# Kernel optimization log

Measured on AMD Instinct MI355X. Metric: run time of the kernel, lower is better.

## Reference

```python
import jax, jax.numpy as jnp
import numpy as np

CHANNELS = 32


def _mlp(x, W1, b1, W2, b2, W3, b3):
    # FNN: Linear -> ReLU -> Linear -> ReLU -> Linear (last layer linear)
    h = jax.nn.relu(x @ W1 + b1)
    h = jax.nn.relu(h @ W2 + b2)
    return h @ W3 + b3


def setup_inputs() -> dict:
    key = jax.random.key(0)
    ks = jax.random.split(key, 8)
    E = 262144
    C = CHANNELS
    H = 128
    d_in = 4  # 2 * spatial_dim
    d_out = C * (C + 1)  # 1056
    s = lambda fan_in: 1.0 / np.sqrt(fan_in)
    return {
        "pos_i": jax.random.normal(ks[0], (E, 2), jnp.float32),
        "pos_j": jax.random.normal(ks[1], (E, 2), jnp.float32),
        "v_j": jax.random.normal(ks[2], (E, C), jnp.float32),
        "W1": jax.random.normal(ks[3], (d_in, H), jnp.float32) * s(d_in),
        "b1": jnp.zeros((H,), jnp.float32),
        "W2": jax.random.normal(ks[4], (H, H), jnp.float32) * s(H),
        "b2": jnp.zeros((H,), jnp.float32),
        "W3": jax.random.normal(ks[5], (H, d_out), jnp.float32) * s(H),
        "b3": jnp.zeros((d_out,), jnp.float32),
    }


def reference(pos_i, pos_j, v_j, W1, b1, W2, b2, W3, b3):
    C = CHANNELS
    pos_ij = jnp.concatenate((pos_i, pos_j), axis=-1)          # [E, 2*spatial_dim]
    kernel = _mlp(pos_ij, W1, b1, W2, b2, W3, b3)
    kernel = kernel.reshape(-1, C, C + 1)                      # [E, C, C+1]
    mat, bias = kernel[..., :, :-1], kernel[..., :, -1]        # [E,C,C], [E,C]
    return jnp.einsum('eij,ej->ei', mat, v_j) + bias           # [E, C]
```

## Files before the change

kernel.cpp:

```cpp
#include <hip/hip_runtime.h>


#define E_TOTAL 262144
#define EPB 256
#define NBLK (E_TOTAL / EPB)

typedef float f32x4 __attribute__((ext_vector_type(4)));
typedef short s8v  __attribute__((ext_vector_type(8)));
typedef short s4v  __attribute__((ext_vector_type(4)));
typedef unsigned int u32;

__device__ __forceinline__ unsigned short f2bf(float x) {
  unsigned u = __float_as_uint(x);
  u += 0x7fffu + ((u >> 16) & 1u);
  return (unsigned short)(u >> 16);
}

__device__ __forceinline__ void ld16_g2l(const void* g, void* l) {
  __builtin_amdgcn_global_load_lds((const __attribute__((address_space(1))) u32*)g,
                                   (__attribute__((address_space(3))) u32*)l, 16, 0, 0);
}

__global__ void prep_pack(const float* __restrict__ W2, const float* __restrict__ W3,
                          const float* __restrict__ b3,
                          unsigned short* __restrict__ Wg2, unsigned short* __restrict__ W2f,
                          unsigned short* __restrict__ b3f, float* __restrict__ b3c) {
  int idx = blockIdx.x * 256 + threadIdx.x;
  if (idx < 135168) {
    int k = idx / 1056, c = idx % 1056;
    int i = c / 33, jc = c % 33;
    int col = jc * 32 + i;
    int nnt = col >> 4, low = col & 15;
    int nn = (nnt & 1) ? (33 + (nnt >> 1)) : (nnt >> 1);
    int ks = k >> 5, kr = k & 31;
    int lane = ((kr >> 3) << 4) + low;
    int jj = k & 7;
    Wg2[((nn * 4 + ks) * 64 + lane) * 8 + jj] = f2bf(W3[idx]);
  }
  if (idx < 16384) {
    int k = idx >> 7, n = idx & 127;
    int ks = k >> 5, kr = k & 31;
    int nt = n >> 4, low = n & 15;
    int l = ((kr >> 3) << 4) + low;
    int jj = k & 7;
    W2f[((ks * 8 + nt) * 64 + l) * 8 + jj] = f2bf(W2[idx]);
  }
  if (idx < 1024) {
    int jj = idx & 7, lane = (idx >> 3) & 63, ih = idx >> 9;
    int j = ((lane >> 4) << 3) + jj, i = ih * 16 + (lane & 15);
    b3f[idx] = f2bf(b3[i * 33 + j]);
  }
  if (idx < 32) b3c[idx] = b3[idx * 33 + 32];
}

template <int IH>
__device__ __forceinline__ void tile_compute(const unsigned short* __restrict__ buf, int t,
                                             const float* __restrict__ vt, int j,
                                             int w, int q, int lane,
                                             const s8v (&af)[2][4], float (&oa)[2][2][4]) {
  const f32x4 zero4 = {0.f, 0.f, 0.f, 0.f};
  s8v bfr[4];
#pragma unroll
  for (int ks = 0; ks < 4; ++ks)
    bfr[ks] = *(const s8v*)&buf[(t * 4 + ks) * 512 + lane * 8];
  const float* vp = vt + j * 260 + w * 32 + q * 4;
#pragma unroll
  for (int m = 0; m < 2; ++m) {
    f32x4 p = __builtin_amdgcn_mfma_f32_16x16x32_bf16(af[m][0], bfr[0], zero4, 0, 0, 0);
#pragma unroll
    for (int ks = 1; ks < 4; ++ks)
      p = __builtin_amdgcn_mfma_f32_16x16x32_bf16(af[m][ks], bfr[ks], p, 0, 0, 0);
    f32x4 vv = *(const f32x4*)(vp + m * 16);
#pragma unroll
    for (int r = 0; r < 4; ++r) oa[IH][m][r] += vv[r] * p[r];
  }
}

__global__ __launch_bounds__(512, 4) void fnn_fused(
    const float* __restrict__ pos_i, const float* __restrict__ pos_j,
    const float* __restrict__ vj, const float* __restrict__ W1,
    const float* __restrict__ b1, const float* __restrict__ b2,
    const unsigned short* __restrict__ W2f, const unsigned short* __restrict__ Wg2,
    const unsigned short* __restrict__ b3f, const float* __restrict__ b3c,
    float* __restrict__ out) {
  __shared__ __attribute__((aligned(16))) char smem[51200];
  float* vt = (float*)smem;
  unsigned short* h1c = (unsigned short*)smem;
  unsigned short* h2n = (unsigned short*)(smem + 17408);
  unsigned short* Bb  = (unsigned short*)(smem + 34816);
  char* BbChar = smem + 34816;

  const int tid = threadIdx.x;
  const int w = tid >> 6, lane = tid & 63, q = lane >> 4, ln = lane & 15;
  const int B0 = blockIdx.x * EPB;

  const int hh0 = (tid & 31) * 4;
  float w1r[4][4], b1r4[4];
#pragma unroll
  for (int d = 0; d < 4; ++d)
#pragma unroll
    for (int u = 0; u < 4; ++u) w1r[d][u] = W1[d * 128 + hh0 + u];
#pragma unroll
  for (int u = 0; u < 4; ++u) b1r4[u] = b1[hh0 + u];

  s8v af[2][4];
  for (int qtr = 0; qtr < 4; ++qtr) {
#pragma unroll
    for (int half = 0; half < 4; ++half) {
      int ee = (tid >> 5) + half * 16;
      int eg = B0 + qtr * 64 + ee;
      float2 pi = *(const float2*)(pos_i + (size_t)eg * 2);
      float2 pj = *(const float2*)(pos_j + (size_t)eg * 2);
      s4v hv;
#pragma unroll
      for (int u = 0; u < 4; ++u) {
        float o = b1r4[u] + pi.x * w1r[0][u] + pi.y * w1r[1][u] +
                  pj.x * w1r[2][u] + pj.y * w1r[3][u];
        hv[u] = (short)f2bf(fmaxf(o, 0.f));
      }
      *(s4v*)&h1c[ee * 136 + hh0] = hv;
    }
    __syncthreads();

#pragma unroll
    for (int s = 0; s < 4; ++s) {
      int tt = w * 4 + s, mt = tt >> 3, nt = tt & 7;
      f32x4 a4 = {0.f, 0.f, 0.f, 0.f};
#pragma unroll
      for (int ks = 0; ks < 4; ++ks) {
        s8v afr = *(const s8v*)&h1c[(mt * 16 + ln) * 136 + ks * 32 + q * 8];
        s8v bfr = *(const s8v*)(W2f + ((ks * 8 + nt) * 64 + lane) * 8);
        a4 = __builtin_amdgcn_mfma_f32_16x16x32_bf16(afr, bfr, a4, 0, 0, 0);
      }
      float b2v = b2[nt * 16 + ln];
      int eb = mt * 16 + q * 4;
      int kc = nt * 16 + ln;
#pragma unroll
      for (int r = 0; r < 4; ++r)
        h2n[(eb + r) * 136 + kc] = f2bf(fmaxf(a4[r] + b2v, 0.f));
    }
    __syncthreads();

    if ((w >> 1) == qtr) {
#pragma unroll
      for (int m = 0; m < 2; ++m)
#pragma unroll
        for (int ks = 0; ks < 4; ++ks)
          af[m][ks] = *(const s8v*)&h2n[(((w & 1) * 32 + m * 16 + ln)) * 136 + ks * 32 + q * 8];
    }
  }

  {
    const unsigned short* src = Wg2 + tid * 8;
    char* dstb = BbChar + w * 1024;
    ld16_g2l(src, dstb);
  }
  __syncthreads();

  float oa[2][2][4];
  {
    s8v av[2];
#pragma unroll
    for (int m = 0; m < 2; ++m) {
      int e = B0 + w * 32 + m * 16 + ln;
      const float4 va = *(const float4*)(vj + (size_t)e * 32 + q * 8);
      const float4 vb = *(const float4*)(vj + (size_t)e * 32 + q * 8 + 4);
      s8v t;
      t[0] = (short)f2bf(va.x); t[1] = (short)f2bf(va.y);
      t[2] = (short)f2bf(va.z); t[3] = (short)f2bf(va.w);
      t[4] = (short)f2bf(vb.x); t[5] = (short)f2bf(vb.y);
      t[6] = (short)f2bf(vb.z); t[7] = (short)f2bf(vb.w);
      av[m] = t;
    }
#pragma unroll
    for (int ih = 0; ih < 2; ++ih) {
      s8v b3fr = *(const s8v*)(b3f + (ih * 64 + lane) * 8);
      float cbv = b3c[ih * 16 + ln];
      f32x4 ci = {cbv, cbv, cbv, cbv};
#pragma unroll
      for (int m = 0; m < 2; ++m) {
        f32x4 p = __builtin_amdgcn_mfma_f32_16x16x32_bf16(av[m], b3fr, ci, 0, 0, 0);
#pragma unroll
        for (int r = 0; r < 4; ++r) oa[ih][m][r] = p[r];
      }
    }
  }

  if (tid < 256) {
    const float* vrow = vj + (size_t)(B0 + tid) * 32;
#pragma unroll
    for (int j4 = 0; j4 < 8; ++j4) {
      float4 vv = *(const float4*)(vrow + j4 * 4);
      vt[(j4 * 4 + 0) * 260 + tid] = vv.x;
      vt[(j4 * 4 + 1) * 260 + tid] = vv.y;
      vt[(j4 * 4 + 2) * 260 + tid] = vv.z;
      vt[(j4 * 4 + 3) * 260 + tid] = vv.w;
    }
    vt[32 * 260 + tid] = 1.0f;
  }
  __syncthreads();

#pragma unroll 1
  for (int c = 0; c < 16; ++c) {
    const unsigned short* buf = Bb + (c & 1) * 4096;
    {
      const unsigned short* src = Wg2 + (size_t)(c + 1) * 4096 + tid * 8;
      char* dstb = BbChar + ((c + 1) & 1) * 8192 + w * 1024;
      ld16_g2l(src, dstb);
    }
    tile_compute<0>(buf, 0, vt, 2 * c,     w, q, lane, af, oa);
    tile_compute<0>(buf, 1, vt, 2 * c + 1, w, q, lane, af, oa);
    __syncthreads();
  }
  {
    const unsigned short* buf = Bb;
    {
      const unsigned short* src = Wg2 + (size_t)17 * 4096 + tid * 8;
      char* dstb = BbChar + 8192 + w * 1024;
      ld16_g2l(src, dstb);
    }
    tile_compute<0>(buf, 0, vt, 32, w, q, lane, af, oa);
    tile_compute<1>(buf, 1, vt, 0,  w, q, lane, af, oa);
    __syncthreads();
  }
#pragma unroll 1
  for (int c = 17; c < 33; ++c) {
    const unsigned short* buf = Bb + (c & 1) * 4096;
    if (c < 32) {
      const unsigned short* src = Wg2 + (size_t)(c + 1) * 4096 + tid * 8;
      char* dstb = BbChar + ((c + 1) & 1) * 8192 + w * 1024;
      ld16_g2l(src, dstb);
    }
    tile_compute<1>(buf, 0, vt, 2 * c - 33, w, q, lane, af, oa);
    tile_compute<1>(buf, 1, vt, 2 * c - 32, w, q, lane, af, oa);
    __syncthreads();
  }

#pragma unroll
  for (int m = 0; m < 2; ++m)
#pragma unroll
    for (int ih = 0; ih < 2; ++ih)
#pragma unroll
      for (int r = 0; r < 4; ++r) {
        int e = B0 + w * 32 + m * 16 + q * 4 + r;
        out[(size_t)e * 32 + ih * 16 + ln] = oa[ih][m][r];
      }
}

extern "C" void kernel_launch(void* const* d_in, const int* in_sizes, int n_in,
                              void* d_out, int out_size, void* d_ws, size_t ws_size,
                              hipStream_t stream) {
  const float* pos_i = (const float*)d_in[0];
  const float* pos_j = (const float*)d_in[1];
  const float* vj    = (const float*)d_in[2];
  const float* W1    = (const float*)d_in[3];
  const float* b1    = (const float*)d_in[4];
  const float* W2    = (const float*)d_in[5];
  const float* b2    = (const float*)d_in[6];
  const float* W3    = (const float*)d_in[7];
  const float* b3    = (const float*)d_in[8];
  float* outp = (float*)d_out;

  unsigned short* Wg2 = (unsigned short*)d_ws;
  unsigned short* W2f = (unsigned short*)((char*)d_ws + 270336);
  unsigned short* b3f = (unsigned short*)((char*)d_ws + 303104);
  float*          b3c = (float*)((char*)d_ws + 305152);

  prep_pack<<<528, 256, 0, stream>>>(W2, W3, b3, Wg2, W2f, b3f, b3c);
  fnn_fused<<<NBLK, 512, 0, stream>>>(pos_i, pos_j, vj, W1, b1, b2, W2f, Wg2, b3f, b3c, outp);
}
```

Baseline: 205.7 us.

## Cut register pressure: stage W1/b1 in LDS, split output accumulators by half

```diff
diff --git a/kernel.cpp b/kernel.cpp
--- a/kernel.cpp
+++ b/kernel.cpp
@@ -53,27 +53,69 @@
   if (idx < 32) b3c[idx] = b3[idx * 33 + 32];
 }
 
-template <int IH>
 __device__ __forceinline__ void tile_compute(const unsigned short* __restrict__ buf, int t,
-                                             const float* __restrict__ vt, int j,
-                                             int w, int q, int lane,
-                                             const s8v (&af)[2][4], float (&oa)[2][2][4]) {
+                                             const float* __restrict__ vp0, int j,
+                                             int lane,
+                                             const s8v (&af)[2][4], float (&oa)[2][4]) {
   const f32x4 zero4 = {0.f, 0.f, 0.f, 0.f};
-  s8v bfr[4];
-#pragma unroll
-  for (int ks = 0; ks < 4; ++ks)
-    bfr[ks] = *(const s8v*)&buf[(t * 4 + ks) * 512 + lane * 8];
-  const float* vp = vt + j * 260 + w * 32 + q * 4;
+  f32x4 p0, p1;
+  {
+    s8v bA = *(const s8v*)&buf[(t * 4 + 0) * 512 + lane * 8];
+    s8v bB = *(const s8v*)&buf[(t * 4 + 1) * 512 + lane * 8];
+    p0 = __builtin_amdgcn_mfma_f32_16x16x32_bf16(af[0][0], bA, zero4, 0, 0, 0);
+    p1 = __builtin_amdgcn_mfma_f32_16x16x32_bf16(af[1][0], bA, zero4, 0, 0, 0);
+    p0 = __builtin_amdgcn_mfma_f32_16x16x32_bf16(af[0][1], bB, p0, 0, 0, 0);
+    p1 = __builtin_amdgcn_mfma_f32_16x16x32_bf16(af[1][1], bB, p1, 0, 0, 0);
+  }
+  {
+    s8v bA = *(const s8v*)&buf[(t * 4 + 2) * 512 + lane * 8];
+    s8v bB = *(const s8v*)&buf[(t * 4 + 3) * 512 + lane * 8];
+    p0 = __builtin_amdgcn_mfma_f32_16x16x32_bf16(af[0][2], bA, p0, 0, 0, 0);
+    p1 = __builtin_amdgcn_mfma_f32_16x16x32_bf16(af[1][2], bA, p1, 0, 0, 0);
+    p0 = __builtin_amdgcn_mfma_f32_16x16x32_bf16(af[0][3], bB, p0, 0, 0, 0);
+    p1 = __builtin_amdgcn_mfma_f32_16x16x32_bf16(af[1][3], bB, p1, 0, 0, 0);
+  }
+  const float* vp = vp0 + j * 260;
+  f32x4 vv0 = *(const f32x4*)(vp);
+  f32x4 vv1 = *(const f32x4*)(vp + 16);
+#pragma unroll
+  for (int r = 0; r < 4; ++r) oa[0][r] += vv0[r] * p0[r];
+#pragma unroll
+  for (int r = 0; r < 4; ++r) oa[1][r] += vv1[r] * p1[r];
+}
+
+__device__ __forceinline__ void init_oa8(float (&oa)[2][4], const float* __restrict__ vj,
+                                         const unsigned short* __restrict__ b3f,
+                                         const float* __restrict__ b3c,
+                                         int B0, int w, int q, int ln, int lane, int ih) {
+  s8v b3fr = *(const s8v*)(b3f + (ih * 64 + lane) * 8);
+  float cbv = b3c[ih * 16 + ln];
+  f32x4 ci = {cbv, cbv, cbv, cbv};
 #pragma unroll
   for (int m = 0; m < 2; ++m) {
-    f32x4 p = __builtin_amdgcn_mfma_f32_16x16x32_bf16(af[m][0], bfr[0], zero4, 0, 0, 0);
-#pragma unroll
-    for (int ks = 1; ks < 4; ++ks)
-      p = __builtin_amdgcn_mfma_f32_16x16x32_bf16(af[m][ks], bfr[ks], p, 0, 0, 0);
-    f32x4 vv = *(const f32x4*)(vp + m * 16);
-#pragma unroll
-    for (int r = 0; r < 4; ++r) oa[IH][m][r] += vv[r] * p[r];
-  }
+    int e = B0 + w * 32 + m * 16 + ln;
+    const float4 va = *(const float4*)(vj + (size_t)e * 32 + q * 8);
+    const float4 vb = *(const float4*)(vj + (size_t)e * 32 + q * 8 + 4);
+    s8v t;
+    t[0] = (short)f2bf(va.x); t[1] = (short)f2bf(va.y);
+    t[2] = (short)f2bf(va.z); t[3] = (short)f2bf(va.w);
+    t[4] = (short)f2bf(vb.x); t[5] = (short)f2bf(vb.y);
+    t[6] = (short)f2bf(vb.z); t[7] = (short)f2bf(vb.w);
+    f32x4 p = __builtin_amdgcn_mfma_f32_16x16x32_bf16(t, b3fr, ci, 0, 0, 0);
+#pragma unroll
+    for (int r = 0; r < 4; ++r) oa[m][r] = p[r];
+  }
+}
+
+__device__ __forceinline__ void store_half8(float* __restrict__ out, const float (&oa)[2][4],
+                                            int B0, int w, int q, int ln, int ih) {
+#pragma unroll
+  for (int m = 0; m < 2; ++m)
+#pragma unroll
+    for (int r = 0; r < 4; ++r) {
+      int e = B0 + w * 32 + m * 16 + q * 4 + r;
+      out[(size_t)e * 32 + ih * 16 + ln] = oa[m][r];
+    }
 }
 
 __global__ __launch_bounds__(512, 4) void fnn_fused(
@@ -83,25 +125,24 @@
     const unsigned short* __restrict__ W2f, const unsigned short* __restrict__ Wg2,
     const unsigned short* __restrict__ b3f, const float* __restrict__ b3c,
     float* __restrict__ out) {
-  __shared__ __attribute__((aligned(16))) char smem[51200];
+  __shared__ __attribute__((aligned(16))) char smem[53760];
   float* vt = (float*)smem;
   unsigned short* h1c = (unsigned short*)smem;
   unsigned short* h2n = (unsigned short*)(smem + 17408);
   unsigned short* Bb  = (unsigned short*)(smem + 34816);
   char* BbChar = smem + 34816;
+  float* w1L = (float*)(smem + 51200);
+  float* b1L = (float*)(smem + 53248);
 
   const int tid = threadIdx.x;
   const int w = tid >> 6, lane = tid & 63, q = lane >> 4, ln = lane & 15;
   const int B0 = blockIdx.x * EPB;
 
+  w1L[tid] = W1[tid];
+  if (tid < 128) b1L[tid] = b1[tid];
+  __syncthreads();
+
   const int hh0 = (tid & 31) * 4;
-  float w1r[4][4], b1r4[4];
-#pragma unroll
-  for (int d = 0; d < 4; ++d)
-#pragma unroll
-    for (int u = 0; u < 4; ++u) w1r[d][u] = W1[d * 128 + hh0 + u];
-#pragma unroll
-  for (int u = 0; u < 4; ++u) b1r4[u] = b1[hh0 + u];
 
   s8v af[2][4];
   for (int qtr = 0; qtr < 4; ++qtr) {
@@ -111,11 +152,15 @@
       int eg = B0 + qtr * 64 + ee;
       float2 pi = *(const float2*)(pos_i + (size_t)eg * 2);
       float2 pj = *(const float2*)(pos_j + (size_t)eg * 2);
+      f32x4 w0 = *(volatile const f32x4*)&w1L[0 * 128 + hh0];
+      f32x4 w1v = *(volatile const f32x4*)&w1L[1 * 128 + hh0];
+      f32x4 w2v = *(volatile const f32x4*)&w1L[2 * 128 + hh0];
+      f32x4 w3v = *(volatile const f32x4*)&w1L[3 * 128 + hh0];
+      f32x4 bb = *(volatile const f32x4*)&b1L[hh0];
       s4v hv;
 #pragma unroll
       for (int u = 0; u < 4; ++u) {
-        float o = b1r4[u] + pi.x * w1r[0][u] + pi.y * w1r[1][u] +
-                  pj.x * w1r[2][u] + pj.y * w1r[3][u];
+        float o = bb[u] + pi.x * w0[u] + pi.y * w1v[u] + pj.x * w2v[u] + pj.y * w3v[u];
         hv[u] = (short)f2bf(fmaxf(o, 0.f));
       }
       *(s4v*)&h1c[ee * 136 + hh0] = hv;
@@ -157,34 +202,8 @@
   }
   __syncthreads();
 
-  float oa[2][2][4];
-  {
-    s8v av[2];
-#pragma unroll
-    for (int m = 0; m < 2; ++m) {
-      int e = B0 + w * 32 + m * 16 + ln;
-      const float4 va = *(const float4*)(vj + (size_t)e * 32 + q * 8);
-      const float4 vb = *(const float4*)(vj + (size_t)e * 32 + q * 8 + 4);
-      s8v t;
-      t[0] = (short)f2bf(va.x); t[1] = (short)f2bf(va.y);
-      t[2] = (short)f2bf(va.z); t[3] = (short)f2bf(va.w);
-      t[4] = (short)f2bf(vb.x); t[5] = (short)f2bf(vb.y);
-      t[6] = (short)f2bf(vb.z); t[7] = (short)f2bf(vb.w);
-      av[m] = t;
-    }
-#pragma unroll
-    for (int ih = 0; ih < 2; ++ih) {
-      s8v b3fr = *(const s8v*)(b3f + (ih * 64 + lane) * 8);
-      float cbv = b3c[ih * 16 + ln];
-      f32x4 ci = {cbv, cbv, cbv, cbv};
-#pragma unroll
-      for (int m = 0; m < 2; ++m) {
-        f32x4 p = __builtin_amdgcn_mfma_f32_16x16x32_bf16(av[m], b3fr, ci, 0, 0, 0);
-#pragma unroll
-        for (int r = 0; r < 4; ++r) oa[ih][m][r] = p[r];
-      }
-    }
-  }
+  float oa[2][4];
+  init_oa8(oa, vj, b3f, b3c, B0, w, q, ln, lane, 0);
 
   if (tid < 256) {
     const float* vrow = vj + (size_t)(B0 + tid) * 32;
@@ -199,6 +218,8 @@
     vt[32 * 260 + tid] = 1.0f;
   }
   __syncthreads();
+
+  const float* vp0 = vt + w * 32 + q * 4;
 
 #pragma unroll 1
   for (int c = 0; c < 16; ++c) {
@@ -208,8 +229,8 @@
       char* dstb = BbChar + ((c + 1) & 1) * 8192 + w * 1024;
       ld16_g2l(src, dstb);
     }
-    tile_compute<0>(buf, 0, vt, 2 * c,     w, q, lane, af, oa);
-    tile_compute<0>(buf, 1, vt, 2 * c + 1, w, q, lane, af, oa);
+    tile_compute(buf, 0, vp0, 2 * c,     lane, af, oa);
+    tile_compute(buf, 1, vp0, 2 * c + 1, lane, af, oa);
     __syncthreads();
   }
   {
@@ -219,8 +240,10 @@
       char* dstb = BbChar + 8192 + w * 1024;
       ld16_g2l(src, dstb);
     }
-    tile_compute<0>(buf, 0, vt, 32, w, q, lane, af, oa);
-    tile_compute<1>(buf, 1, vt, 0,  w, q, lane, af, oa);
+    tile_compute(buf, 0, vp0, 32, lane, af, oa);
+    store_half8(out, oa, B0, w, q, ln, 0);
+    init_oa8(oa, vj, b3f, b3c, B0, w, q, ln, lane, 1);
+    tile_compute(buf, 1, vp0, 0, lane, af, oa);
     __syncthreads();
   }
 #pragma unroll 1
@@ -231,20 +254,11 @@
       char* dstb = BbChar + ((c + 1) & 1) * 8192 + w * 1024;
       ld16_g2l(src, dstb);
     }
-    tile_compute<1>(buf, 0, vt, 2 * c - 33, w, q, lane, af, oa);
-    tile_compute<1>(buf, 1, vt, 2 * c - 32, w, q, lane, af, oa);
-    __syncthreads();
-  }
-
-#pragma unroll
-  for (int m = 0; m < 2; ++m)
-#pragma unroll
-    for (int ih = 0; ih < 2; ++ih)
-#pragma unroll
-      for (int r = 0; r < 4; ++r) {
-        int e = B0 + w * 32 + m * 16 + q * 4 + r;
-        out[(size_t)e * 32 + ih * 16 + ln] = oa[ih][m][r];
-      }
+    tile_compute(buf, 0, vp0, 2 * c - 33, lane, af, oa);
+    tile_compute(buf, 1, vp0, 2 * c - 32, lane, af, oa);
+    __syncthreads();
+  }
+  store_half8(out, oa, B0, w, q, ln, 1);
 }
 
 extern "C" void kernel_launch(void* const* d_in, const int* in_sizes, int n_in,
```

Measured after the change: 217.1 us. +5.5%, slower.
